# Kernel tuning notes

Measured on AMD Instinct MI355X. Metric: run time of the kernel, lower is better.

Reference implementation:

```python
import jax, jax.numpy as jnp
import numpy as np

NUM_CLASSES = 100


def setup_inputs() -> dict:
    key = jax.random.key(0)
    k1, k2, k3, k4 = jax.random.split(key, 4)
    x = jax.random.normal(k1, (256, 2048), dtype=jnp.float32)
    W_model = jax.random.normal(k2, (2048, 64), dtype=jnp.float32)
    database_code = jax.random.normal(k3, (100000, 64), dtype=jnp.float32)
    database_labels = jax.random.randint(k4, (100000,), 0, NUM_CLASSES, dtype=jnp.int64)
    return {
        "x": x,
        "W_model": W_model,
        "database_code": database_code,
        "database_labels": database_labels,
        "K": 1000,
    }


def reference(x, W_model, database_code, database_labels, K):
    # model(x): single linear projection to hash-code space [B, d]
    out = x @ W_model
    # sim_score = out @ codes.T * -0.5 + num_classes/2  -> [B, N]
    sim = jnp.matmul(out, database_code.T) * -0.5 + NUM_CLASSES / 2
    # np.argpartition(sim, K)[:, :K] selects the K SMALLEST scores.
    # Equivalent set via top_k on negated scores.
    _, topk_idx = jax.lax.top_k(-sim, K)            # [B, K]
    topk_labels = database_labels[topk_idx]          # [B, K]
    # per-class histogram over the top-K retrieved labels
    classes = jnp.arange(NUM_CLASSES, dtype=topk_labels.dtype)
    counts = (topk_labels[:, :, None] == classes[None, None, :]).sum(axis=1)  # [B, C]
    probs = counts.astype(jnp.float32) / K
    return probs
```

## Files before the change

### kernel.cpp

```cpp
#include <hip/hip_runtime.h>
#include <hip/hip_fp16.h>


#define NBK 256
#define FNB 1024
#define CAPC 2048
#define BCAP 2048
#define MROWS 32
#define NCHX 64
#define NCLS 100

typedef _Float16 half8 __attribute__((ext_vector_type(8)));
typedef float floatx4 __attribute__((ext_vector_type(4)));

static __device__ __forceinline__ unsigned packh2(float a, float b) {
  _Float16 ha = (_Float16)a, hb = (_Float16)b;
  unsigned short ua, ub;
  __builtin_memcpy(&ua, &ha, 2); __builtin_memcpy(&ub, &hb, 2);
  return (unsigned)ua | ((unsigned)ub << 16);
}

static __device__ __forceinline__ void rowRange(double b1sq, double cmax,
                                                double& lo, double& inv, double& bw) {
  double hr = 0.5 * sqrt(b1sq * cmax) * 1.000001 + 9.0;
  lo = 50.0 - hr;
  bw = (2.0 * hr) / (double)NBK;
  inv = (double)NBK / (2.0 * hr);
}

static __device__ __forceinline__ void loadA(const unsigned short* __restrict__ out16,
                                             int m0, int mr, int quad,
                                             half8& a00, half8& a01, half8& a10, half8& a11) {
  const uint4* o4 = (const uint4*)out16;
  uint4 u;
  u = o4[(size_t)(m0 + mr) * 8 + quad];          __builtin_memcpy(&a00, &u, 16);
  u = o4[(size_t)(m0 + mr) * 8 + 4 + quad];      __builtin_memcpy(&a01, &u, 16);
  u = o4[(size_t)(m0 + 16 + mr) * 8 + quad];     __builtin_memcpy(&a10, &u, 16);
  u = o4[(size_t)(m0 + 16 + mr) * 8 + 4 + quad]; __builtin_memcpy(&a11, &u, 16);
}

__global__ __launch_bounds__(1024) void k_prep(const float* __restrict__ x,
                                               const float* __restrict__ W,
                                               const float* __restrict__ codes,
                                               const int* __restrict__ labels,
                                               int N, int Npad, int D, int B, int nCvt,
                                               unsigned short* __restrict__ codes16,
                                               float* __restrict__ cmaxSlab,
                                               double* __restrict__ out64,
                                               unsigned short* __restrict__ out16,
                                               double* __restrict__ B1sq,
                                               int* __restrict__ shiftp) {
  __shared__ double red[1024];
  __shared__ float xs[2048];
  __shared__ float fredw[16];
  __shared__ int flag;
  int blk = (int)blockIdx.x, tid = (int)threadIdx.x;
  int lane = tid & 63, wid = tid >> 6;
  if (blk < nCvt) {
    int gl = tid & 15, g = tid >> 4;
    int base = blk * 256;
    int r0 = base + g, r1 = base + 64 + g, r2 = base + 128 + g, r3 = base + 192 + g;
    float4 q0 = {0.f,0.f,0.f,0.f}, q1 = q0, q2 = q0, q3 = q0;
    if (r0 < N) q0 = ((const float4*)(codes + (size_t)r0 * 64))[gl];
    if (r1 < N) q1 = ((const float4*)(codes + (size_t)r1 * 64))[gl];
    if (r2 < N) q2 = ((const float4*)(codes + (size_t)r2 * 64))[gl];
    if (r3 < N) q3 = ((const float4*)(codes + (size_t)r3 * 64))[gl];
    uint2 o0, o1, o2, o3;
    o0.x = packh2(q0.x, q0.y); o0.y = packh2(q0.z, q0.w);
    o1.x = packh2(q1.x, q1.y); o1.y = packh2(q1.z, q1.w);
    o2.x = packh2(q2.x, q2.y); o2.y = packh2(q2.z, q2.w);
    o3.x = packh2(q3.x, q3.y); o3.y = packh2(q3.z, q3.w);
    ((uint2*)(codes16 + (size_t)r0 * 64))[gl] = o0;
    ((uint2*)(codes16 + (size_t)r1 * 64))[gl] = o1;
    ((uint2*)(codes16 + (size_t)r2 * 64))[gl] = o2;
    ((uint2*)(codes16 + (size_t)r3 * 64))[gl] = o3;
    float bmax = 0.0f;
#define NRM(qv)                                                            \
    { double c2 = fma((double)(qv).x, (double)(qv).x, 0.0);                \
      c2 = fma((double)(qv).y, (double)(qv).y, c2);                        \
      c2 = fma((double)(qv).z, (double)(qv).z, c2);                        \
      c2 = fma((double)(qv).w, (double)(qv).w, c2);                        \
      c2 += __shfl_xor(c2, 1, 16); c2 += __shfl_xor(c2, 2, 16);            \
      c2 += __shfl_xor(c2, 4, 16); c2 += __shfl_xor(c2, 8, 16);            \
      bmax = fmaxf(bmax, (float)(c2 * 1.000001)); }
    NRM(q0) NRM(q1) NRM(q2) NRM(q3)
#undef NRM
#pragma unroll
    for (int off = 32; off > 0; off >>= 1) bmax = fmaxf(bmax, __shfl_xor(bmax, off, 64));
    if (lane == 0) fredw[wid] = bmax;
    __syncthreads();
    if (tid == 0) {
      float m = fredw[0];
#pragma unroll
      for (int j = 1; j < 16; ++j) m = fmaxf(m, fredw[j]);
      cmaxSlab[blk] = m;
    }
  } else if (blk < nCvt + B) {
    int b = blk - nCvt;
    const float* xr = x + (size_t)b * D;
    for (int i = tid; i < (D >> 1); i += 1024)
      ((float2*)xs)[i] = ((const float2*)xr)[i];
    __syncthreads();
    int t = tid & 63, w = tid >> 6;
    int kc = D >> 4;
    int k0 = w * kc;
    double a[8];
#pragma unroll
    for (int j = 0; j < 8; ++j) a[j] = 0.0;
#pragma unroll 2
    for (int k = k0; k < k0 + kc; k += 8) {
#pragma unroll
      for (int j = 0; j < 8; ++j)
        a[j] = fma((double)xs[k + j], (double)W[(size_t)(k + j) * 64 + t], a[j]);
    }
    red[tid] = ((a[0] + a[1]) + (a[2] + a[3])) + ((a[4] + a[5]) + (a[6] + a[7]));
    __syncthreads();
    if (w == 0) {
      double o = 0.0;
#pragma unroll
      for (int j = 0; j < 16; ++j) o += red[t + 64 * j];
      out64[(size_t)b * 64 + t] = o;
      _Float16 h = (_Float16)(float)o;
      unsigned short us; __builtin_memcpy(&us, &h, 2);
      out16[(size_t)b * 64 + t] = us;
      double sq = o * o;
#pragma unroll
      for (int off = 1; off < 64; off <<= 1) sq += __shfl_xor(sq, off, 64);
      if (t == 0) B1sq[b] = sq;
    }
  } else {
    if (tid == 0) flag = 0;
    __syncthreads();
    int m = N < 256 ? N : 256;
    if (tid < m && labels[2 * tid + 1] != 0) atomicOr(&flag, 1);
    __syncthreads();
    if (tid == 0) *shiftp = flag ? 0 : 1;
  }
}

__global__ __launch_bounds__(512) void k_mhist(const unsigned short* __restrict__ codes16,
                                               const unsigned short* __restrict__ out16,
                                               const double* __restrict__ B1sq,
                                               const float* __restrict__ cmaxSlab,
                                               int nCvt, int N, int Npad, int cpb, int B,
                                               unsigned short* __restrict__ histg,
                                               unsigned char* __restrict__ buck) {
  __shared__ unsigned hist[MROWS * NBK];
  __shared__ float sP[MROWS], sQ[MROWS], fredw[8];
  int tid = (int)threadIdx.x;
  int lane = tid & 63, wv = tid >> 6;
  int m0 = (int)blockIdx.y * MROWS, cx = (int)blockIdx.x;
  {
    float m = 0.0f;
    for (int i = tid; i < nCvt; i += 512) m = fmaxf(m, cmaxSlab[i]);
#pragma unroll
    for (int off = 32; off > 0; off >>= 1) m = fmaxf(m, __shfl_xor(m, off, 64));
    if (lane == 0) fredw[wv] = m;
  }
  for (int i = tid; i < MROWS * NBK; i += 512) hist[i] = 0u;
  __syncthreads();
  float cmax;
  { float m = fredw[0];
#pragma unroll
    for (int j = 1; j < 8; ++j) m = fmaxf(m, fredw[j]);
    cmax = m; }
  if (tid < MROWS) {
    double lo, inv, bw;
    rowRange(B1sq[m0 + tid], (double)cmax, lo, inv, bw);
    sP[tid] = (float)(-0.5 * inv);
    sQ[tid] = (float)((50.0 - lo) * inv);
  }
  __syncthreads();
  int quad = lane >> 4, mr = lane & 15;
  half8 a00, a01, a10, a11;
  loadA(out16, m0, mr, quad, a00, a01, a10, a11);
  float P0[4], Q0[4], P1[4], Q1[4];
#pragma unroll
  for (int r = 0; r < 4; ++r) {
    P0[r] = sP[quad*4 + r];      Q0[r] = sQ[quad*4 + r];
    P1[r] = sP[16 + quad*4 + r]; Q1[r] = sQ[16 + quad*4 + r];
  }
  int cstart = cx * cpb;
  int cend = cstart + cpb; if (cend > N) cend = N;
  const uint4* c4 = (const uint4*)codes16;
  floatx4 z = {0.f, 0.f, 0.f, 0.f};
  for (int base = cstart; base < cend; base += 128) {
    int nrow = base + wv * 16 + mr;
    int nc = nrow < Npad ? nrow : Npad - 1;
    uint4 ub0 = c4[(size_t)nc * 8 + quad];
    uint4 ub1 = c4[(size_t)nc * 8 + 4 + quad];
    half8 b0, b1;
    __builtin_memcpy(&b0, &ub0, 16); __builtin_memcpy(&b1, &ub1, 16);
    floatx4 d0 = __builtin_amdgcn_mfma_f32_16x16x32_f16(a00, b0, z, 0, 0, 0);
    d0 = __builtin_amdgcn_mfma_f32_16x16x32_f16(a01, b1, d0, 0, 0, 0);
    floatx4 d1 = __builtin_amdgcn_mfma_f32_16x16x32_f16(a10, b0, z, 0, 0, 0);
    d1 = __builtin_amdgcn_mfma_f32_16x16x32_f16(a11, b1, d1, 0, 0, 0);
    if (nrow < N) {
#pragma unroll
      for (int r = 0; r < 4; ++r) {
        int bk0 = (int)fmaf(d0[r], P0[r], Q0[r]);
        bk0 = bk0 < 0 ? 0 : (bk0 > NBK-1 ? NBK-1 : bk0);
        atomicAdd(&hist[(quad*4 + r) * NBK + bk0], 1u);
        buck[(size_t)(m0 + quad*4 + r) * N + nrow] = (unsigned char)bk0;
        int bk1 = (int)fmaf(d1[r], P1[r], Q1[r]);
        bk1 = bk1 < 0 ? 0 : (bk1 > NBK-1 ? NBK-1 : bk1);
        atomicAdd(&hist[(16 + quad*4 + r) * NBK + bk1], 1u);
        buck[(size_t)(m0 + 16 + quad*4 + r) * N + nrow] = (unsigned char)bk1;
      }
    }
  }
  __syncthreads();
  for (int i = tid; i < MROWS * NBK; i += 512)
    histg[((size_t)cx * B + (m0 + (i >> 8))) * NBK + (i & (NBK - 1))] =
        (unsigned short)hist[i];
}

__global__ __launch_bounds__(1024) void k_rowfinal(const float* __restrict__ codes,
                                                   const double* __restrict__ out64,
                                                   const double* __restrict__ B1sq,
                                                   const float* __restrict__ cmaxSlab,
                                                   const unsigned short* __restrict__ histg,
                                                   const unsigned char* __restrict__ buck,
                                                   const int* __restrict__ labels,
                                                   const int* __restrict__ shiftp,
                                                   const int* __restrict__ Kp,
                                                   float* __restrict__ outp,
                                                   int nCvt, int N, int B) {
  __shared__ float fredw[16];
  __shared__ unsigned sp[1024];
  __shared__ unsigned s[NBK];
  __shared__ unsigned wtot[4];
  __shared__ double key[CAPC];
  __shared__ int kidx[CAPC];
  __shared__ int blist[BCAP];
  __shared__ unsigned fhist[FNB];
  __shared__ unsigned ftot[16];
  __shared__ unsigned short tlist[CAPC];
  __shared__ double sod[64];
  __shared__ unsigned lab[NCLS];
  __shared__ unsigned ccnt, bcnt, tcnt, sCntLt;
  __shared__ int sTb, sFtb;
  int b = (int)blockIdx.x, tid = (int)threadIdx.x;
  int lane = tid & 63, wid = tid >> 6;

  {
    float m = (tid < nCvt) ? cmaxSlab[tid] : 0.0f;
    for (int i = tid + 1024; i < nCvt; i += 1024) m = fmaxf(m, cmaxSlab[i]);
#pragma unroll
    for (int off = 32; off > 0; off >>= 1) m = fmaxf(m, __shfl_xor(m, off, 64));
    if (lane == 0) fredw[wid] = m;
  }
  fhist[tid] = 0u;
  if (tid < 64) sod[tid] = out64[(size_t)b * 64 + tid];
  if (tid < NCLS) lab[tid] = 0u;
  if (tid == 0) { ccnt = 0u; bcnt = 0u; tcnt = 0u; sCntLt = 0u; sFtb = FNB; }
  __syncthreads();
  float cmax;
  { float m = fredw[0];
#pragma unroll
    for (int j = 1; j < 16; ++j) m = fmaxf(m, fredw[j]);
    cmax = m; }

  {
    int bk = tid & 255, cq = tid >> 8;
    unsigned part = 0;
#pragma unroll
    for (int t2 = 0; t2 < 16; ++t2)
      part += (unsigned)histg[((size_t)(cq * 16 + t2) * B + b) * NBK + bk];
    sp[tid] = part;
  }
  __syncthreads();
  {
    unsigned v = 0;
    if (tid < 256) {
      v = sp[tid] + sp[tid + 256] + sp[tid + 512] + sp[tid + 768];
#pragma unroll
      for (int off = 1; off < 64; off <<= 1) {
        unsigned t = (unsigned)__shfl_up((int)v, off, 64);
        if (lane >= off) v += t;
      }
      if (lane == 63) wtot[wid] = v;
    }
    __syncthreads();
    if (tid < 256) {
      for (int j = 0; j < wid; ++j) v += wtot[j];
      s[tid] = v;
    }
  }
  __syncthreads();
  unsigned K = (unsigned)Kp[0];
  if (tid < 256) {
    unsigned prev = tid ? s[tid - 1] : 0u;
    if (s[tid] >= K && prev < K) sTb = tid;
  }
  __syncthreads();
  int tb = sTb;
  double lo, inv, bwd;
  rowRange(B1sq[b], (double)cmax, lo, inv, bwd);
  double S = sqrt(B1sq[b] * (double)cmax);
  double Mtot = 2.0 * (0.5 * S * 1.1e-3 + 0.05) + 1e-3;
  int q = (int)ceil(Mtot / bwd);
  int belowMax = tb - 1 - q;
  int candMax = tb + 1 + q;
  if (candMax > NBK - 1) candMax = NBK - 1;
  unsigned btot = (belowMax >= 0) ? s[belowMax] : 0u;
  int shift = *shiftp;

  {
    const uint4* bw16 = (const uint4*)(buck + (size_t)b * N);
    int nw16 = N >> 4;
    bool fast = (candMax <= 127);
    unsigned c1x = (unsigned)(candMax + 1) * 0x01010101u;
#define CLS1(nn, bkv)                                                  \
    { int bk_ = (int)(bkv);                                            \
      if (bk_ <= belowMax) {                                           \
        unsigned p_ = atomicAdd(&bcnt, 1u);                            \
        if (p_ < BCAP) blist[p_] = (nn);                               \
      } else if (bk_ <= candMax) {                                     \
        unsigned p_ = atomicAdd(&ccnt, 1u);                            \
        if (p_ < CAPC) kidx[p_] = (nn);                                \
      } }
#define PROCW(w_, nb)                                                  \
    if (!fast || (((w_) - c1x) & ~(w_) & 0x80808080u)) {               \
      CLS1((nb)+0, (w_) & 0xFF)         CLS1((nb)+1, ((w_) >> 8) & 0xFF) \
      CLS1((nb)+2, ((w_) >> 16) & 0xFF) CLS1((nb)+3, (w_) >> 24)       \
    }
    for (int i = tid; i < nw16; i += 2048) {
      uint4 v0 = bw16[i];
      int i1 = i + 1024; bool h1 = i1 < nw16;
      uint4 v1 = {0u, 0u, 0u, 0u};
      if (h1) v1 = bw16[i1];
      int nb0 = i << 4;
      PROCW(v0.x, nb0) PROCW(v0.y, nb0 + 4) PROCW(v0.z, nb0 + 8) PROCW(v0.w, nb0 + 12)
      if (h1) {
        int nb1 = i1 << 4;
        PROCW(v1.x, nb1) PROCW(v1.y, nb1 + 4) PROCW(v1.z, nb1 + 8) PROCW(v1.w, nb1 + 12)
      }
    }
#undef PROCW
    for (int n = (nw16 << 4) + tid; n < N; n += 1024) {
      CLS1(n, buck[(size_t)b * N + n])
    }
#undef CLS1
  }
  __syncthreads();

  {
    int bm = (int)bcnt; if (bm > BCAP) bm = BCAP;
    for (int i = tid; i < bm; i += 1024)
      atomicAdd(&lab[labels[(size_t)blist[i] << shift]], 1u);
  }
  int cc = (int)ccnt; if (cc > CAPC) cc = CAPC;
  {
    int g = tid >> 4, gl = tid & 15;
    for (int i = g; i < cc; i += 64) {
      int n = kidx[i];
      float4 qv = ((const float4*)(codes + (size_t)n * 64))[gl];
      double p = fma((double)qv.x, sod[gl*4+0], 0.0);
      p = fma((double)qv.y, sod[gl*4+1], p);
      p = fma((double)qv.z, sod[gl*4+2], p);
      p = fma((double)qv.w, sod[gl*4+3], p);
      p += __shfl_xor(p, 1, 16);
      p += __shfl_xor(p, 2, 16);
      p += __shfl_xor(p, 4, 16);
      p += __shfl_xor(p, 8, 16);
      if (gl == 0) key[i] = fma(p, -0.5, 50.0);
    }
  }
  __syncthreads();

  int need = (int)K - (int)btot;
  double fLo = lo + (double)(belowMax + 1) * bwd - Mtot;
  double fInv = (double)FNB / ((double)(candMax - belowMax) * bwd + 2.0 * Mtot);
  for (int i = tid; i < cc; i += 1024) {
    int fb = (int)((key[i] - fLo) * fInv);
    fb = fb < 0 ? 0 : (fb > FNB - 1 ? FNB - 1 : fb);
    atomicAdd(&fhist[fb], 1u);
  }
  __syncthreads();
  {
    unsigned v = fhist[tid];
#pragma unroll
    for (int off = 1; off < 64; off <<= 1) {
      unsigned t = (unsigned)__shfl_up((int)v, off, 64);
      if (lane >= off) v += t;
    }
    if (lane == 63) ftot[wid] = v;
    sp[tid] = v;
  }
  __syncthreads();
  {
    unsigned off = 0;
    for (int j = 0; j < wid; ++j) off += ftot[j];
    unsigned ci = sp[tid] + off;
    unsigned ce = ci - fhist[tid];
    if ((int)ci >= need && (int)ce < need) { sFtb = tid; sCntLt = ce; }
  }
  __syncthreads();
  int ftb = sFtb;
  for (int i = tid; i < cc; i += 1024) {
    int fb = (int)((key[i] - fLo) * fInv);
    fb = fb < 0 ? 0 : (fb > FNB - 1 ? FNB - 1 : fb);
    if (fb < ftb) {
      atomicAdd(&lab[labels[(size_t)kidx[i] << shift]], 1u);
    } else if (fb == ftb) {
      unsigned p_ = atomicAdd(&tcnt, 1u);
      if (p_ < CAPC) tlist[p_] = (unsigned short)i;
    }
  }
  __syncthreads();
  {
    int tn = (int)tcnt; if (tn > CAPC) tn = CAPC;
    int rem = need - (int)sCntLt;
    for (int j = tid; j < tn; j += 1024) {
      int i = (int)tlist[j];
      double ki = key[i]; int ii = kidx[i];
      int rank = 0;
      for (int j2 = 0; j2 < tn; ++j2) {
        int i2 = (int)tlist[j2];
        double k2 = key[i2];
        rank += (k2 < ki || (k2 == ki && kidx[i2] < ii)) ? 1 : 0;
      }
      if (rank < rem) atomicAdd(&lab[labels[(size_t)ii << shift]], 1u);
    }
  }
  __syncthreads();
  double Kd = (double)K;
  for (int c = tid; c < NCLS; c += 1024)
    outp[b * NCLS + c] = (float)((double)lab[c] / Kd);
}

extern "C" void kernel_launch(void* const* d_in, const int* in_sizes, int n_in,
                              void* d_out, int out_size, void* d_ws, size_t ws_size,
                              hipStream_t stream) {
  const float* x     = (const float*)d_in[0];
  const float* W     = (const float*)d_in[1];
  const float* codes = (const float*)d_in[2];
  const int* labels  = (const int*)d_in[3];
  const int* Kp      = (const int*)d_in[4];

  const int B = out_size / NCLS;
  const int N = in_sizes[3];
  const int D = in_sizes[0] / B;
  const int Npad = (N + 255) & ~255;
  const int cpb = (((N + NCHX - 1) / NCHX) + 127) & ~127;
  const int nCvt = Npad / 256;

  char* p = (char*)d_ws;
  double* out64      = (double*)p;   p += (size_t)B * 64 * sizeof(double);
  unsigned short* out16 = (unsigned short*)p; p += (size_t)B * 64 * 2;
  double* B1sq       = (double*)p;   p += (size_t)B * sizeof(double);
  int* shiftp        = (int*)p;      p += 64;
  float* cmaxSlab    = (float*)p;    p += 4096;
  unsigned short* histg = (unsigned short*)p; p += (size_t)NCHX * B * NBK * 2;
  unsigned char* buck   = (unsigned char*)p;  p += (size_t)B * N;
  unsigned short* codes16 = (unsigned short*)p;

  k_prep<<<nCvt + B + 1, 1024, 0, stream>>>(x, W, codes, labels, N, Npad, D, B, nCvt,
                                            codes16, cmaxSlab, out64, out16, B1sq, shiftp);
  k_mhist<<<dim3(NCHX, B / MROWS), 512, 0, stream>>>(codes16, out16, B1sq, cmaxSlab,
                                                     nCvt, N, Npad, cpb, B, histg, buck);
  k_rowfinal<<<B, 1024, 0, stream>>>(codes, out64, B1sq, cmaxSlab, histg, buck,
                                     labels, shiftp, Kp, (float*)d_out, nCvt, N, B);
}
```

Baseline: 152.7 us.

## Add per-16-element bucket minimum summary to skip scanning bucket bytes

The histogram kernel now reduces each row's 16-element group of bucket indices to its minimum with shuffles and writes it to a new gmin array. The final per-row kernel scans this summary first and reads the full bucket bytes only for groups whose minimum falls within the candidate range, cutting global reads of the bucket array. The exact-rescoring loop is also unrolled by two to overlap code fetches. In exchange the histogram kernel does extra shuffles and stores, and the group scan may diverge more.

```diff
diff --git a/kernel.cpp b/kernel.cpp
--- a/kernel.cpp
+++ b/kernel.cpp
@@ -144,12 +144,14 @@
                                                const float* __restrict__ cmaxSlab,
                                                int nCvt, int N, int Npad, int cpb, int B,
                                                unsigned short* __restrict__ histg,
-                                               unsigned char* __restrict__ buck) {
+                                               unsigned char* __restrict__ buck,
+                                               unsigned char* __restrict__ gmin) {
   __shared__ unsigned hist[MROWS * NBK];
   __shared__ float sP[MROWS], sQ[MROWS], fredw[8];
   int tid = (int)threadIdx.x;
   int lane = tid & 63, wv = tid >> 6;
   int m0 = (int)blockIdx.y * MROWS, cx = (int)blockIdx.x;
+  int N16g = (N + 15) >> 4;
   {
     float m = 0.0f;
     for (int i = tid; i < nCvt; i += 512) m = fmaxf(m, cmaxSlab[i]);
@@ -195,17 +197,34 @@
     d0 = __builtin_amdgcn_mfma_f32_16x16x32_f16(a01, b1, d0, 0, 0, 0);
     floatx4 d1 = __builtin_amdgcn_mfma_f32_16x16x32_f16(a10, b0, z, 0, 0, 0);
     d1 = __builtin_amdgcn_mfma_f32_16x16x32_f16(a11, b1, d1, 0, 0, 0);
-    if (nrow < N) {
-#pragma unroll
-      for (int r = 0; r < 4; ++r) {
-        int bk0 = (int)fmaf(d0[r], P0[r], Q0[r]);
-        bk0 = bk0 < 0 ? 0 : (bk0 > NBK-1 ? NBK-1 : bk0);
+    int gidx = (base >> 4) + wv;
+    bool gok = (gidx < N16g);
+#pragma unroll
+    for (int r = 0; r < 4; ++r) {
+      int bk0 = (int)fmaf(d0[r], P0[r], Q0[r]);
+      bk0 = bk0 < 0 ? 0 : (bk0 > NBK-1 ? NBK-1 : bk0);
+      int bk1 = (int)fmaf(d1[r], P1[r], Q1[r]);
+      bk1 = bk1 < 0 ? 0 : (bk1 > NBK-1 ? NBK-1 : bk1);
+      if (nrow < N) {
         atomicAdd(&hist[(quad*4 + r) * NBK + bk0], 1u);
         buck[(size_t)(m0 + quad*4 + r) * N + nrow] = (unsigned char)bk0;
-        int bk1 = (int)fmaf(d1[r], P1[r], Q1[r]);
-        bk1 = bk1 < 0 ? 0 : (bk1 > NBK-1 ? NBK-1 : bk1);
         atomicAdd(&hist[(16 + quad*4 + r) * NBK + bk1], 1u);
         buck[(size_t)(m0 + 16 + quad*4 + r) * N + nrow] = (unsigned char)bk1;
+      }
+      int v0 = nrow < N ? bk0 : 255;
+      int v1 = nrow < N ? bk1 : 255;
+      int t0;
+      t0 = __shfl_xor(v0, 1, 16); v0 = v0 < t0 ? v0 : t0;
+      t0 = __shfl_xor(v0, 2, 16); v0 = v0 < t0 ? v0 : t0;
+      t0 = __shfl_xor(v0, 4, 16); v0 = v0 < t0 ? v0 : t0;
+      t0 = __shfl_xor(v0, 8, 16); v0 = v0 < t0 ? v0 : t0;
+      t0 = __shfl_xor(v1, 1, 16); v1 = v1 < t0 ? v1 : t0;
+      t0 = __shfl_xor(v1, 2, 16); v1 = v1 < t0 ? v1 : t0;
+      t0 = __shfl_xor(v1, 4, 16); v1 = v1 < t0 ? v1 : t0;
+      t0 = __shfl_xor(v1, 8, 16); v1 = v1 < t0 ? v1 : t0;
+      if (mr == 0 && gok) {
+        gmin[(size_t)(m0 + quad*4 + r) * N16g + gidx] = (unsigned char)v0;
+        gmin[(size_t)(m0 + 16 + quad*4 + r) * N16g + gidx] = (unsigned char)v1;
       }
     }
   }
@@ -221,6 +240,7 @@
                                                    const float* __restrict__ cmaxSlab,
                                                    const unsigned short* __restrict__ histg,
                                                    const unsigned char* __restrict__ buck,
+                                                   const unsigned char* __restrict__ gmin,
                                                    const int* __restrict__ labels,
                                                    const int* __restrict__ shiftp,
                                                    const int* __restrict__ Kp,
@@ -307,8 +327,9 @@
   int shift = *shiftp;
 
   {
-    const uint4* bw16 = (const uint4*)(buck + (size_t)b * N);
-    int nw16 = N >> 4;
+    int N16g = (N + 15) >> 4;
+    const unsigned char* gmr = gmin + (size_t)b * N16g;
+    const unsigned char* br  = buck + (size_t)b * N;
     bool fast = (candMax <= 127);
     unsigned c1x = (unsigned)(candMax + 1) * 0x01010101u;
 #define CLS1(nn, bkv)                                                  \
@@ -320,27 +341,38 @@
         unsigned p_ = atomicAdd(&ccnt, 1u);                            \
         if (p_ < CAPC) kidx[p_] = (nn);                                \
       } }
-#define PROCW(w_, nb)                                                  \
-    if (!fast || (((w_) - c1x) & ~(w_) & 0x80808080u)) {               \
-      CLS1((nb)+0, (w_) & 0xFF)         CLS1((nb)+1, ((w_) >> 8) & 0xFF) \
-      CLS1((nb)+2, ((w_) >> 16) & 0xFF) CLS1((nb)+3, (w_) >> 24)       \
-    }
-    for (int i = tid; i < nw16; i += 2048) {
-      uint4 v0 = bw16[i];
-      int i1 = i + 1024; bool h1 = i1 < nw16;
-      uint4 v1 = {0u, 0u, 0u, 0u};
-      if (h1) v1 = bw16[i1];
-      int nb0 = i << 4;
-      PROCW(v0.x, nb0) PROCW(v0.y, nb0 + 4) PROCW(v0.z, nb0 + 8) PROCW(v0.w, nb0 + 12)
-      if (h1) {
-        int nb1 = i1 << 4;
-        PROCW(v1.x, nb1) PROCW(v1.y, nb1 + 4) PROCW(v1.z, nb1 + 8) PROCW(v1.w, nb1 + 12)
+#define DOGRP(g_)                                                      \
+    { int n0_ = (g_) << 4;                                             \
+      if (n0_ + 15 < N) {                                              \
+        uint4 v_ = *(const uint4*)(br + n0_);                          \
+        unsigned u_;                                                   \
+        u_ = v_.x; CLS1(n0_+0,  u_ & 0xFF) CLS1(n0_+1,  (u_>>8)&0xFF)  \
+                   CLS1(n0_+2,  (u_>>16)&0xFF) CLS1(n0_+3,  u_>>24)    \
+        u_ = v_.y; CLS1(n0_+4,  u_ & 0xFF) CLS1(n0_+5,  (u_>>8)&0xFF)  \
+                   CLS1(n0_+6,  (u_>>16)&0xFF) CLS1(n0_+7,  u_>>24)    \
+        u_ = v_.z; CLS1(n0_+8,  u_ & 0xFF) CLS1(n0_+9,  (u_>>8)&0xFF)  \
+                   CLS1(n0_+10, (u_>>16)&0xFF) CLS1(n0_+11, u_>>24)    \
+        u_ = v_.w; CLS1(n0_+12, u_ & 0xFF) CLS1(n0_+13, (u_>>8)&0xFF)  \
+                   CLS1(n0_+14, (u_>>16)&0xFF) CLS1(n0_+15, u_>>24)    \
+      } else {                                                         \
+        for (int k_ = n0_; k_ < N; ++k_) CLS1(k_, br[k_])              \
+      } }
+    int nw4 = N16g >> 2;
+    for (int i = tid; i < nw4; i += 1024) {
+      unsigned w = *(const unsigned*)(gmr + 4 * i);
+      bool any = fast ? (((w - c1x) & ~w & 0x80808080u) != 0) : true;
+      if (any) {
+#pragma unroll
+        for (int j = 0; j < 4; ++j) {
+          int gb = (int)((w >> (8 * j)) & 0xFFu);
+          if (gb <= candMax) DOGRP(4 * i + j)
+        }
       }
     }
-#undef PROCW
-    for (int n = (nw16 << 4) + tid; n < N; n += 1024) {
-      CLS1(n, buck[(size_t)b * N + n])
-    }
+    for (int g = (nw4 << 2) + tid; g < N16g; g += 1024) {
+      if ((int)gmr[g] <= candMax) DOGRP(g)
+    }
+#undef DOGRP
 #undef CLS1
   }
   __syncthreads();
@@ -353,18 +385,28 @@
   int cc = (int)ccnt; if (cc > CAPC) cc = CAPC;
   {
     int g = tid >> 4, gl = tid & 15;
-    for (int i = g; i < cc; i += 64) {
-      int n = kidx[i];
-      float4 qv = ((const float4*)(codes + (size_t)n * 64))[gl];
-      double p = fma((double)qv.x, sod[gl*4+0], 0.0);
-      p = fma((double)qv.y, sod[gl*4+1], p);
-      p = fma((double)qv.z, sod[gl*4+2], p);
-      p = fma((double)qv.w, sod[gl*4+3], p);
-      p += __shfl_xor(p, 1, 16);
-      p += __shfl_xor(p, 2, 16);
-      p += __shfl_xor(p, 4, 16);
-      p += __shfl_xor(p, 8, 16);
-      if (gl == 0) key[i] = fma(p, -0.5, 50.0);
+    for (int i = g; i < cc; i += 128) {
+      int i1 = i + 64; bool h1 = i1 < cc;
+      int n0 = kidx[i];
+      int n1 = h1 ? kidx[i1] : n0;
+      float4 qv0 = ((const float4*)(codes + (size_t)n0 * 64))[gl];
+      float4 qv1 = ((const float4*)(codes + (size_t)n1 * 64))[gl];
+      double p0 = fma((double)qv0.x, sod[gl*4+0], 0.0);
+      p0 = fma((double)qv0.y, sod[gl*4+1], p0);
+      p0 = fma((double)qv0.z, sod[gl*4+2], p0);
+      p0 = fma((double)qv0.w, sod[gl*4+3], p0);
+      double p1 = fma((double)qv1.x, sod[gl*4+0], 0.0);
+      p1 = fma((double)qv1.y, sod[gl*4+1], p1);
+      p1 = fma((double)qv1.z, sod[gl*4+2], p1);
+      p1 = fma((double)qv1.w, sod[gl*4+3], p1);
+      p0 += __shfl_xor(p0, 1, 16); p1 += __shfl_xor(p1, 1, 16);
+      p0 += __shfl_xor(p0, 2, 16); p1 += __shfl_xor(p1, 2, 16);
+      p0 += __shfl_xor(p0, 4, 16); p1 += __shfl_xor(p1, 4, 16);
+      p0 += __shfl_xor(p0, 8, 16); p1 += __shfl_xor(p1, 8, 16);
+      if (gl == 0) {
+        key[i] = fma(p0, -0.5, 50.0);
+        if (h1) key[i1] = fma(p1, -0.5, 50.0);
+      }
     }
   }
   __syncthreads();
@@ -445,6 +487,7 @@
   const int Npad = (N + 255) & ~255;
   const int cpb = (((N + NCHX - 1) / NCHX) + 127) & ~127;
   const int nCvt = Npad / 256;
+  const int N16g = (N + 15) >> 4;
 
   char* p = (char*)d_ws;
   double* out64      = (double*)p;   p += (size_t)B * 64 * sizeof(double);
@@ -454,12 +497,13 @@
   float* cmaxSlab    = (float*)p;    p += 4096;
   unsigned short* histg = (unsigned short*)p; p += (size_t)NCHX * B * NBK * 2;
   unsigned char* buck   = (unsigned char*)p;  p += (size_t)B * N;
+  unsigned char* gmin   = (unsigned char*)p;  p += ((size_t)B * N16g + 63) & ~63ull;
   unsigned short* codes16 = (unsigned short*)p;
 
   k_prep<<<nCvt + B + 1, 1024, 0, stream>>>(x, W, codes, labels, N, Npad, D, B, nCvt,
                                             codes16, cmaxSlab, out64, out16, B1sq, shiftp);
   k_mhist<<<dim3(NCHX, B / MROWS), 512, 0, stream>>>(codes16, out16, B1sq, cmaxSlab,
-                                                     nCvt, N, Npad, cpb, B, histg, buck);
-  k_rowfinal<<<B, 1024, 0, stream>>>(codes, out64, B1sq, cmaxSlab, histg, buck,
+                                                     nCvt, N, Npad, cpb, B, histg, buck, gmin);
+  k_rowfinal<<<B, 1024, 0, stream>>>(codes, out64, B1sq, cmaxSlab, histg, buck, gmin,
                                      labels, shiftp, Kp, (float*)d_out, nCvt, N, B);
 }
```

Result: slower. 166.4 us (+9.0%).
